# Kernel tuning notes

Hardware: AMD Instinct MI355X
Metric: run time of the kernel (lower is better)

The kernel has to match this reference:

```python
import jax, jax.numpy as jnp
import numpy as np

N_HEADS = 8
NEG_INF = -1e9


def setup_inputs() -> dict:
    key = jax.random.key(0)
    ks = jax.random.split(key, 9)
    B, S, D = 4, 2048, 512
    scale = 1.0 / np.sqrt(D)
    x = jax.random.normal(ks[0], (B, S, D), dtype=jnp.float32)
    mask = jnp.tril(jnp.ones((S, S), dtype=bool))[None, None, :, :]  # causal [1,1,S,S]
    W_Q_w = jax.random.normal(ks[1], (D, D), dtype=jnp.float32) * scale
    W_Q_b = jax.random.normal(ks[2], (D,), dtype=jnp.float32) * 0.02
    W_K_w = jax.random.normal(ks[3], (D, D), dtype=jnp.float32) * scale
    W_K_b = jax.random.normal(ks[4], (D,), dtype=jnp.float32) * 0.02
    W_V_w = jax.random.normal(ks[5], (D, D), dtype=jnp.float32) * scale
    W_V_b = jax.random.normal(ks[6], (D,), dtype=jnp.float32) * 0.02
    W_O_w = jax.random.normal(ks[7], (D, D), dtype=jnp.float32) * scale
    W_O_b = jax.random.normal(ks[8], (D,), dtype=jnp.float32) * 0.02
    return {"x": x, "mask": mask,
            "W_Q_w": W_Q_w, "W_Q_b": W_Q_b, "W_K_w": W_K_w, "W_K_b": W_K_b,
            "W_V_w": W_V_w, "W_V_b": W_V_b, "W_O_w": W_O_w, "W_O_b": W_O_b}


def reference(x, mask, W_Q_w, W_Q_b, W_K_w, W_K_b, W_V_w, W_V_b, W_O_w, W_O_b):
    B, S, D = x.shape
    H = N_HEADS
    Dh = D // H
    # projections (torch Linear: x @ W.T + b), split heads -> [B,H,S,Dh]
    def split_heads(t):
        return t.reshape(B, S, H, Dh).transpose(0, 2, 1, 3)
    Q = split_heads(x @ W_Q_w.T + W_Q_b)
    K = split_heads(x @ W_K_w.T + W_K_b)
    V = split_heads(x @ W_V_w.T + W_V_b)
    # scaled dot-product attention with explicit [B,H,S,S] scores
    scores = jnp.einsum("bhqd,bhkd->bhqk", Q, K) / jnp.sqrt(jnp.float32(Dh))
    scores = jnp.where(mask, scores, jnp.float32(NEG_INF))
    att = jax.nn.softmax(scores, axis=-1)
    out = jnp.einsum("bhqk,bhkd->bhqd", att, V)
    out = out.transpose(0, 2, 1, 3).reshape(B, S, D)
    return out @ W_O_w.T + W_O_b
```

## Files before the change

kernel.cpp:

```cpp
#include <hip/hip_runtime.h>
#include <hip/hip_bf16.h>

#define BATCH 4
#define SEQ   2048
#define DIM   512
#define NH    8
#define DH    64
#define NTOK  (BATCH*SEQ)

typedef __bf16 bf16x8 __attribute__((ext_vector_type(8)));
typedef float  f32x4  __attribute__((ext_vector_type(4)));

#define MFMA16(a,b,c) __builtin_amdgcn_mfma_f32_16x16x32_bf16((a),(b),(c),0,0,0)

#if __has_builtin(__builtin_amdgcn_exp2f)
#define EXP2F(x) __builtin_amdgcn_exp2f(x)
#else
#define EXP2F(x) exp2f(x)
#endif

#define QSCALE 0.18033688011112042f
#define SMAX 16.0f

typedef __attribute__((address_space(1))) void GAS;
typedef __attribute__((address_space(3))) void LAS;
__device__ __forceinline__ void gl_lds16(const void* g, void* l) {
  __builtin_amdgcn_global_load_lds((GAS*)g, (LAS*)l, 16, 0, 0);
}

__global__ __launch_bounds__(256) void cvt_f32_bf16(const float* __restrict__ src,
                                                    __bf16* __restrict__ dst, int n8) {
  int i = blockIdx.x * blockDim.x + threadIdx.x;
  if (i >= n8) return;
  const float4* s = (const float4*)src;
  float4 a = s[2*i], b = s[2*i+1];
  bf16x8 o;
  o[0] = (__bf16)a.x; o[1] = (__bf16)a.y; o[2] = (__bf16)a.z; o[3] = (__bf16)a.w;
  o[4] = (__bf16)b.x; o[5] = (__bf16)b.y; o[6] = (__bf16)b.z; o[7] = (__bf16)b.w;
  *(bf16x8*)&dst[8*i] = o;
}

__global__ __launch_bounds__(256) void cvt_weights(
    const float* __restrict__ s0, const float* __restrict__ s1,
    const float* __restrict__ s2, const float* __restrict__ s3,
    __bf16* __restrict__ o0, __bf16* __restrict__ o1,
    __bf16* __restrict__ o2, __bf16* __restrict__ o3) {
  int i = blockIdx.x * blockDim.x + threadIdx.x;
  const int which = i >> 15, off = i & 32767;
  const float* src = (which == 0) ? s0 : (which == 1) ? s1 : (which == 2) ? s2 : s3;
  __bf16* dst      = (which == 0) ? o0 : (which == 1) ? o1 : (which == 2) ? o2 : o3;
  const float4* s = (const float4*)src;
  float4 a = s[2*off], b = s[2*off+1];
  bf16x8 o;
  o[0] = (__bf16)a.x; o[1] = (__bf16)a.y; o[2] = (__bf16)a.z; o[3] = (__bf16)a.w;
  o[4] = (__bf16)b.x; o[5] = (__bf16)b.y; o[6] = (__bf16)b.z; o[7] = (__bf16)b.w;
  *(bf16x8*)&dst[8*off] = o;
}

__global__ __launch_bounds__(256) void gemm_qkv(
    const __bf16* __restrict__ xb,
    const __bf16* __restrict__ wq, const __bf16* __restrict__ wk,
    const __bf16* __restrict__ wv,
    const float* __restrict__ bq, const float* __restrict__ bk,
    const float* __restrict__ bv,
    __bf16* __restrict__ Qb, __bf16* __restrict__ Kb, __bf16* __restrict__ Vt)
{
  const int z = blockIdx.z;
  const __bf16* W    = (z == 0) ? wq : (z == 1) ? wk : wv;
  const float*  bias = (z == 0) ? bq : (z == 1) ? bk : bv;

  __shared__ __align__(16) __bf16 As[128*64];
  __shared__ __align__(16) __bf16 Bs[128*64];

  const int tid  = threadIdx.x;
  const int m0   = blockIdx.x * 128, n0 = blockIdx.y * 128;
  const int w    = tid >> 6, lane = tid & 63, quad = lane >> 4, l16 = lane & 15;
  const int wm   = (w >> 1) * 64, wn = (w & 1) * 64;
  const int srow = w*32 + (lane >> 3);
  const int scc  = (lane & 7) * 8;

  f32x4 acc[4][4] = {};

  for (int k0 = 0; k0 < DIM; k0 += 64) {
#pragma unroll
    for (int i = 0; i < 4; ++i) {
      const int row = srow + i*8;
      gl_lds16(&xb[(size_t)(m0+row)*DIM + k0 + scc], &As[(w*4+i)*512]);
      gl_lds16(&W [(size_t)(n0+row)*DIM + k0 + scc], &Bs[(w*4+i)*512]);
    }
    __syncthreads();
#pragma unroll
    for (int kk = 0; kk < 2; ++kk) {
      const int ko = kk*32 + quad*8;
      bf16x8 af[4], bfr[4];
#pragma unroll
      for (int f = 0; f < 4; ++f) {
        af[f]  = *(const bf16x8*)&As[(wm + f*16 + l16)*64 + ko];
        bfr[f] = *(const bf16x8*)&Bs[(wn + f*16 + l16)*64 + ko];
      }
#pragma unroll
      for (int fm = 0; fm < 4; ++fm)
#pragma unroll
        for (int fn = 0; fn < 4; ++fn)
          acc[fm][fn] = MFMA16(af[fm], bfr[fn], acc[fm][fn]);
    }
    __syncthreads();
  }

#pragma unroll
  for (int fm = 0; fm < 4; ++fm) {
#pragma unroll
    for (int fn = 0; fn < 4; ++fn) {
      const int col  = n0 + wn + fn*16 + l16;
      const float bc = bias[col];
      const int h = col >> 6, dh = col & 63;
#pragma unroll
      for (int r = 0; r < 4; ++r) {
        const int row = m0 + wm + fm*16 + quad*4 + r;
        const int b = row >> 11, s = row & 2047;
        const float v = acc[fm][fn][r] + bc;
        if (z == 2) {
          Vt[((size_t)(b*NH + h)*DH + dh)*SEQ + s] = (__bf16)v;
        } else if (z == 0) {
          Qb[((size_t)(b*NH + h)*SEQ + s)*DH + dh] = (__bf16)(v * QSCALE);
        } else {
          Kb[((size_t)(b*NH + h)*SEQ + s)*DH + dh] = (__bf16)v;
        }
      }
    }
  }
}

__global__ __launch_bounds__(256) void gemm_out(
    const __bf16* __restrict__ attnb, const __bf16* __restrict__ wo,
    const float* __restrict__ bo, float* __restrict__ out)
{
  __shared__ __align__(16) __bf16 As[128*64];
  __shared__ __align__(16) __bf16 Bs[128*64];

  const int tid = threadIdx.x;
  const int m0  = blockIdx.x * 128, n0 = blockIdx.y * 128;
  const int w   = tid >> 6, lane = tid & 63, quad = lane >> 4, l16 = lane & 15;
  const int wm  = (w >> 1) * 64, wn = (w & 1) * 64;
  const int srow = w*32 + (lane >> 3);
  const int scc  = (lane & 7) * 8;

  f32x4 acc[4][4] = {};

  for (int k0 = 0; k0 < DIM; k0 += 64) {
#pragma unroll
    for (int i = 0; i < 4; ++i) {
      const int row = srow + i*8;
      gl_lds16(&attnb[(size_t)(m0+row)*DIM + k0 + scc], &As[(w*4+i)*512]);
      gl_lds16(&wo   [(size_t)(n0+row)*DIM + k0 + scc], &Bs[(w*4+i)*512]);
    }
    __syncthreads();
#pragma unroll
    for (int kk = 0; kk < 2; ++kk) {
      const int ko = kk*32 + quad*8;
      bf16x8 af[4], bfr[4];
#pragma unroll
      for (int f = 0; f < 4; ++f) {
        af[f]  = *(const bf16x8*)&As[(wm + f*16 + l16)*64 + ko];
        bfr[f] = *(const bf16x8*)&Bs[(wn + f*16 + l16)*64 + ko];
      }
#pragma unroll
      for (int fm = 0; fm < 4; ++fm)
#pragma unroll
        for (int fn = 0; fn < 4; ++fn)
          acc[fm][fn] = MFMA16(af[fm], bfr[fn], acc[fm][fn]);
    }
    __syncthreads();
  }

#pragma unroll
  for (int fm = 0; fm < 4; ++fm) {
#pragma unroll
    for (int fn = 0; fn < 4; ++fn) {
      const int col  = n0 + wn + fn*16 + l16;
      const float bc = bo[col];
#pragma unroll
      for (int r = 0; r < 4; ++r) {
        const int row = m0 + wm + fm*16 + quad*4 + r;
        out[(size_t)row*DIM + col] = acc[fm][fn][r] + bc;
      }
    }
  }
}

__global__ __launch_bounds__(64) void flash_attn(
    const __bf16* __restrict__ Qb, const __bf16* __restrict__ Kb,
    const __bf16* __restrict__ Vt, __bf16* __restrict__ attnb)
{
  const int idx = blockIdx.x;
  const int bh  = idx & 31;
  const int t   = 63 - (idx >> 5);
  const int b   = bh >> 3, h = bh & 7;
  const int lane = threadIdx.x & 63, quad = lane >> 4, l16 = lane & 15;
  const int q0  = t * 32;

  const __bf16* Qp = Qb + (size_t)bh * SEQ * DH;
  const __bf16* Kp = Kb + (size_t)bh * SEQ * DH;
  const __bf16* Vp = Vt + (size_t)bh * DH * SEQ;

  __shared__ __align__(16) __bf16 Pw[32*88];

  bf16x8 qf[2][2];
#pragma unroll
  for (int mf = 0; mf < 2; ++mf)
#pragma unroll
    for (int kk = 0; kk < 2; ++kk)
      qf[mf][kk] = *(const bf16x8*)&Qp[(size_t)(q0 + mf*16 + l16)*DH + kk*32 + quad*8];

  f32x4 of[2][4] = {};
  float l_[2][4];
#pragma unroll
  for (int mf = 0; mf < 2; ++mf)
#pragma unroll
    for (int r = 0; r < 4; ++r) l_[mf][r] = 0.f;

  const int ktiles = (q0 >> 6) + 1;

  bf16x8 kfA[4][2], kfB[4][2];
#pragma unroll
  for (int fn = 0; fn < 4; ++fn)
#pragma unroll
    for (int kk = 0; kk < 2; ++kk)
      kfA[fn][kk] = *(const bf16x8*)&Kp[(size_t)(fn*16 + l16)*DH + kk*32 + quad*8];

#define TILE_STEP(KC, KN, KT)                                                  \
  {                                                                            \
    const int k0 = (KT) * 64;                                                  \
                   \
    bf16x8 vf[4][2];                                                           \
    _Pragma("unroll")                                                          \
    for (int nd = 0; nd < 4; ++nd)                                             \
      _Pragma("unroll")                                                        \
      for (int kq = 0; kq < 2; ++kq)                                           \
        vf[nd][kq] = *(const bf16x8*)&Vp[(size_t)(nd*16 + l16)*SEQ + k0 +      \
                                         kq*32 + quad*8];                      \
                               \
    {                                                                          \
      const int kn0 = ((KT) + 1 < ktiles) ? k0 + 64 : 0;                       \
      _Pragma("unroll")                                                        \
      for (int fn = 0; fn < 4; ++fn)                                           \
        _Pragma("unroll")                                                      \
        for (int kk = 0; kk < 2; ++kk)                                         \
          KN[fn][kk] = *(const bf16x8*)&Kp[(size_t)(kn0 + fn*16 + l16)*DH +    \
                                           kk*32 + quad*8];                    \
    }                                                                          \
                                   \
    f32x4 sf[2][4] = {};                                                       \
    __builtin_amdgcn_s_setprio(1);                                             \
    _Pragma("unroll")                                                          \
    for (int mf = 0; mf < 2; ++mf)                                             \
      _Pragma("unroll")                                                        \
      for (int fn = 0; fn < 4; ++fn) {                                         \
        sf[mf][fn] = MFMA16(qf[mf][0], KC[fn][0], sf[mf][fn]);                 \
        sf[mf][fn] = MFMA16(qf[mf][1], KC[fn][1], sf[mf][fn]);                 \
      }                                                                        \
    __builtin_amdgcn_s_setprio(0);                                             \
                               \
    if (k0 + 63 > q0) {                                                        \
      _Pragma("unroll")                                                        \
      for (int mf = 0; mf < 2; ++mf)                                           \
        _Pragma("unroll")                                                      \
        for (int fn = 0; fn < 4; ++fn) {                                       \
          const int col = k0 + fn*16 + l16;                                    \
          _Pragma("unroll")                                                    \
          for (int r = 0; r < 4; ++r) {                                        \
            const int row = q0 + mf*16 + quad*4 + r;                           \
            if (col > row) sf[mf][fn][r] = -1e30f;                             \
          }                                                                    \
        }                                                                      \
    }                                                                          \
                         \
    _Pragma("unroll")                                                          \
    for (int mf = 0; mf < 2; ++mf)                                             \
      _Pragma("unroll")                                                        \
      for (int fn = 0; fn < 4; ++fn)                                           \
        _Pragma("unroll")                                                      \
        for (int r = 0; r < 4; ++r)                                            \
          sf[mf][fn][r] = EXP2F(sf[mf][fn][r] - SMAX);                         \
    _Pragma("unroll")                                                          \
    for (int mf = 0; mf < 2; ++mf)                                             \
      _Pragma("unroll")                                                        \
      for (int r = 0; r < 4; ++r)                                              \
        l_[mf][r] += (sf[mf][0][r] + sf[mf][1][r]) +                           \
                     (sf[mf][2][r] + sf[mf][3][r]);                            \
                                           \
    _Pragma("unroll")                                                          \
    for (int mf = 0; mf < 2; ++mf)                                             \
      _Pragma("unroll")                                                        \
      for (int fn = 0; fn < 4; ++fn)                                           \
        _Pragma("unroll")                                                      \
        for (int r = 0; r < 4; ++r)                                            \
          Pw[(mf*16 + quad*4 + r)*88 + fn*16 + l16] = (__bf16)sf[mf][fn][r];   \
    bf16x8 pa[2][2];                                                           \
    _Pragma("unroll")                                                          \
    for (int mf = 0; mf < 2; ++mf)                                             \
      _Pragma("unroll")                                                        \
      for (int kq = 0; kq < 2; ++kq)                                           \
        pa[mf][kq] = *(const bf16x8*)&Pw[(mf*16 + l16)*88 + kq*32 + quad*8];   \
                                                      \
    __builtin_amdgcn_s_setprio(1);                                             \
    _Pragma("unroll")                                                          \
    for (int mf = 0; mf < 2; ++mf)                                             \
      _Pragma("unroll")                                                        \
      for (int nd = 0; nd < 4; ++nd) {                                         \
        of[mf][nd] = MFMA16(pa[mf][0], vf[nd][0], of[mf][nd]);                 \
        of[mf][nd] = MFMA16(pa[mf][1], vf[nd][1], of[mf][nd]);                 \
      }                                                                        \
    __builtin_amdgcn_s_setprio(0);                                             \
  }

  for (int kt = 0; kt < ktiles; kt += 2) {
    TILE_STEP(kfA, kfB, kt);
    if (kt + 1 < ktiles) TILE_STEP(kfB, kfA, kt + 1);
  }
#undef TILE_STEP

#pragma unroll
  for (int d = 1; d < 16; d <<= 1)
#pragma unroll
    for (int mf = 0; mf < 2; ++mf)
#pragma unroll
      for (int r = 0; r < 4; ++r)
        l_[mf][r] += __shfl_xor(l_[mf][r], d);
#pragma unroll
  for (int mf = 0; mf < 2; ++mf)
#pragma unroll
    for (int r = 0; r < 4; ++r)
      l_[mf][r] = 1.0f / l_[mf][r];
#pragma unroll
  for (int mf = 0; mf < 2; ++mf)
#pragma unroll
    for (int nd = 0; nd < 4; ++nd) {
      const int dh = nd*16 + l16;
#pragma unroll
      for (int r = 0; r < 4; ++r) {
        const int q = q0 + mf*16 + quad*4 + r;
        attnb[((size_t)b*SEQ + q)*DIM + h*DH + dh] = (__bf16)(of[mf][nd][r] * l_[mf][r]);
      }
    }
}

extern "C" void kernel_launch(void* const* d_in, const int* in_sizes, int n_in,
                              void* d_out, int out_size, void* d_ws, size_t ws_size,
                              hipStream_t stream) {
  const float* x  = (const float*)d_in[0];
  const float* Wq = (const float*)d_in[2];
  const float* bq = (const float*)d_in[3];
  const float* Wk = (const float*)d_in[4];
  const float* bk = (const float*)d_in[5];
  const float* Wv = (const float*)d_in[6];
  const float* bv = (const float*)d_in[7];
  const float* Wo = (const float*)d_in[8];
  const float* bo = (const float*)d_in[9];
  float* out = (float*)d_out;

  __bf16* xb    = (__bf16*)d_ws;
  __bf16* wq    = xb + (size_t)NTOK*DIM;
  __bf16* wk    = wq + DIM*DIM;
  __bf16* wv    = wk + DIM*DIM;
  __bf16* wo    = wv + DIM*DIM;
  __bf16* Qb    = wo + DIM*DIM;
  __bf16* Kb    = Qb + (size_t)NTOK*DIM;
  __bf16* Vt    = Kb + (size_t)NTOK*DIM;
  __bf16* attnb = Vt + (size_t)NTOK*DIM;

  cvt_f32_bf16<<<(NTOK*DIM/8)/256, 256, 0, stream>>>(x, xb, NTOK*DIM/8);
  cvt_weights<<<(4*DIM*DIM/8)/256, 256, 0, stream>>>(Wq, Wk, Wv, Wo, wq, wk, wv, wo);

  gemm_qkv<<<dim3(NTOK/128, DIM/128, 3), 256, 0, stream>>>(
      xb, wq, wk, wv, bq, bk, bv, Qb, Kb, Vt);

  flash_attn<<<2048, 64, 0, stream>>>(Qb, Kb, Vt, attnb);

  gemm_out<<<dim3(NTOK/128, DIM/128), 256, 0, stream>>>(attnb, wo, bo, out);
}
```

Measured before the change: 214.1 us.

## Split long causal query tiles across two KV-range blocks with atomic merge

```diff
diff --git a/kernel.cpp b/kernel.cpp
--- a/kernel.cpp
+++ b/kernel.cpp
@@ -9,6 +9,7 @@
 #define NTOK  (BATCH*SEQ)
 
 typedef __bf16 bf16x8 __attribute__((ext_vector_type(8)));
+typedef __bf16 bf16x4 __attribute__((ext_vector_type(4)));
 typedef float  f32x4  __attribute__((ext_vector_type(4)));
 
 #define MFMA16(a,b,c) __builtin_amdgcn_mfma_f32_16x16x32_bf16((a),(b),(c),0,0,0)
@@ -190,14 +191,32 @@
 
 __global__ __launch_bounds__(64) void flash_attn(
     const __bf16* __restrict__ Qb, const __bf16* __restrict__ Kb,
-    const __bf16* __restrict__ Vt, __bf16* __restrict__ attnb)
+    const __bf16* __restrict__ Vt, __bf16* __restrict__ attnb,
+    float* __restrict__ Of, float* __restrict__ Lb)
 {
   const int idx = blockIdx.x;
   const int bh  = idx & 31;
-  const int t   = 63 - (idx >> 5);
   const int b   = bh >> 3, h = bh & 7;
   const int lane = threadIdx.x & 63, quad = lane >> 4, l16 = lane & 15;
-  const int q0  = t * 32;
+
+  int t, c0tile, c1tile;
+  bool split;
+  if (idx < 2048) {
+    t = 63 - (idx >> 6);
+    const int ktiles = (t >> 1) + 1;
+    const int half   = ktiles >> 1;
+    const int c      = (idx >> 5) & 1;
+    c0tile = c ? half : 0;
+    c1tile = c ? ktiles : half;
+    split  = true;
+  } else {
+    const int li = idx - 2048;
+    t = 31 - (li >> 5);
+    c0tile = 0;
+    c1tile = (t >> 1) + 1;
+    split  = false;
+  }
+  const int q0 = t * 32;
 
   const __bf16* Qp = Qb + (size_t)bh * SEQ * DH;
   const __bf16* Kp = Kb + (size_t)bh * SEQ * DH;
@@ -219,14 +238,12 @@
 #pragma unroll
     for (int r = 0; r < 4; ++r) l_[mf][r] = 0.f;
 
-  const int ktiles = (q0 >> 6) + 1;
-
   bf16x8 kfA[4][2], kfB[4][2];
 #pragma unroll
   for (int fn = 0; fn < 4; ++fn)
 #pragma unroll
     for (int kk = 0; kk < 2; ++kk)
-      kfA[fn][kk] = *(const bf16x8*)&Kp[(size_t)(fn*16 + l16)*DH + kk*32 + quad*8];
+      kfA[fn][kk] = *(const bf16x8*)&Kp[(size_t)(c0tile*64 + fn*16 + l16)*DH + kk*32 + quad*8];
 
 #define TILE_STEP(KC, KN, KT)                                                  \
   {                                                                            \
@@ -241,7 +258,7 @@
                                          kq*32 + quad*8];                      \
                                \
     {                                                                          \
-      const int kn0 = ((KT) + 1 < ktiles) ? k0 + 64 : 0;                       \
+      const int kn0 = ((KT) + 1 < c1tile) ? k0 + 64 : 0;                       \
       _Pragma("unroll")                                                        \
       for (int fn = 0; fn < 4; ++fn)                                           \
         _Pragma("unroll")                                                      \
@@ -314,9 +331,9 @@
     __builtin_amdgcn_s_setprio(0);                                             \
   }
 
-  for (int kt = 0; kt < ktiles; kt += 2) {
+  for (int kt = c0tile; kt < c1tile; kt += 2) {
     TILE_STEP(kfA, kfB, kt);
-    if (kt + 1 < ktiles) TILE_STEP(kfB, kfA, kt + 1);
+    if (kt + 1 < c1tile) TILE_STEP(kfB, kfA, kt + 1);
   }
 #undef TILE_STEP
 
@@ -327,22 +344,62 @@
 #pragma unroll
       for (int r = 0; r < 4; ++r)
         l_[mf][r] += __shfl_xor(l_[mf][r], d);
-#pragma unroll
-  for (int mf = 0; mf < 2; ++mf)
-#pragma unroll
-    for (int r = 0; r < 4; ++r)
-      l_[mf][r] = 1.0f / l_[mf][r];
-#pragma unroll
-  for (int mf = 0; mf < 2; ++mf)
-#pragma unroll
-    for (int nd = 0; nd < 4; ++nd) {
-      const int dh = nd*16 + l16;
-#pragma unroll
-      for (int r = 0; r < 4; ++r) {
-        const int q = q0 + mf*16 + quad*4 + r;
-        attnb[((size_t)b*SEQ + q)*DIM + h*DH + dh] = (__bf16)(of[mf][nd][r] * l_[mf][r]);
-      }
-    }
+
+  if (!split) {
+#pragma unroll
+    for (int mf = 0; mf < 2; ++mf)
+#pragma unroll
+      for (int r = 0; r < 4; ++r)
+        l_[mf][r] = 1.0f / l_[mf][r];
+#pragma unroll
+    for (int mf = 0; mf < 2; ++mf)
+#pragma unroll
+      for (int nd = 0; nd < 4; ++nd) {
+        const int dh = nd*16 + l16;
+#pragma unroll
+        for (int r = 0; r < 4; ++r) {
+          const int q = q0 + mf*16 + quad*4 + r;
+          attnb[((size_t)b*SEQ + q)*DIM + h*DH + dh] = (__bf16)(of[mf][nd][r] * l_[mf][r]);
+        }
+      }
+  } else {
+    const int ro = (bh << 10) + (q0 - 1024);
+    if (l16 == 0) {
+#pragma unroll
+      for (int mf = 0; mf < 2; ++mf)
+#pragma unroll
+        for (int r = 0; r < 4; ++r)
+          atomicAdd(&Lb[ro + mf*16 + quad*4 + r], l_[mf][r]);
+    }
+#pragma unroll
+    for (int mf = 0; mf < 2; ++mf)
+#pragma unroll
+      for (int nd = 0; nd < 4; ++nd) {
+        const int dh = nd*16 + l16;
+#pragma unroll
+        for (int r = 0; r < 4; ++r)
+          atomicAdd(&Of[(size_t)(ro + mf*16 + quad*4 + r)*DH + dh], of[mf][nd][r]);
+      }
+  }
+}
+
+__global__ __launch_bounds__(256) void norm_split(
+    const float* __restrict__ Of, const float* __restrict__ Lb,
+    __bf16* __restrict__ attnb)
+{
+  const int i = blockIdx.x * 256 + threadIdx.x;
+  const int e = i * 4;
+  const int bh  = e >> 16;
+  const int rem = e & 65535;
+  const int row = rem >> 6;
+  const int dh  = rem & 63;
+  const f32x4 v = *(const f32x4*)&Of[e];
+  const float inv = 1.0f / Lb[(bh << 10) + row];
+  bf16x4 o;
+  o[0] = (__bf16)(v[0] * inv); o[1] = (__bf16)(v[1] * inv);
+  o[2] = (__bf16)(v[2] * inv); o[3] = (__bf16)(v[3] * inv);
+  const int b = bh >> 3, h = bh & 7, q = 1024 + row;
+  *(bf16x4*)&attnb[((size_t)b*SEQ + q)*DIM + h*DH + dh] = o;
 }
 
 extern "C" void kernel_launch(void* const* d_in, const int* in_sizes, int n_in,
@@ -369,13 +426,21 @@
   __bf16* Vt    = Kb + (size_t)NTOK*DIM;
   __bf16* attnb = Vt + (size_t)NTOK*DIM;
 
+  float* Of = (float*)xb;
+  float* Lb = (float*)wq;
+
   cvt_f32_bf16<<<(NTOK*DIM/8)/256, 256, 0, stream>>>(x, xb, NTOK*DIM/8);
   cvt_weights<<<(4*DIM*DIM/8)/256, 256, 0, stream>>>(Wq, Wk, Wv, Wo, wq, wk, wv, wo);
 
   gemm_qkv<<<dim3(NTOK/128, DIM/128, 3), 256, 0, stream>>>(
       xb, wq, wk, wv, bq, bk, bv, Qb, Kb, Vt);
 
-  flash_attn<<<2048, 64, 0, stream>>>(Qb, Kb, Vt, attnb);
+  hipMemsetAsync(Of, 0, (size_t)32*1024*64*sizeof(float), stream);
+  hipMemsetAsync(Lb, 0, (size_t)32*1024*sizeof(float), stream);
+
+  flash_attn<<<3072, 64, 0, stream>>>(Qb, Kb, Vt, attnb, Of, Lb);
+
+  norm_split<<<2048, 256, 0, stream>>>(Of, Lb, attnb);
 
   gemm_out<<<dim3(NTOK/128, DIM/128), 256, 0, stream>>>(attnb, wo, bo, out);
 }
```

Measured after the change: 240.4 us. 1.12x slower.

## Stage QKV epilogue through LDS for coalesced stores, merge converts, shrink out-GEMM tile

Applied to the files above, without the earlier changes.

```diff
diff --git a/kernel.cpp b/kernel.cpp
--- a/kernel.cpp
+++ b/kernel.cpp
@@ -28,27 +28,25 @@
   __builtin_amdgcn_global_load_lds((GAS*)g, (LAS*)l, 16, 0, 0);
 }
 
-__global__ __launch_bounds__(256) void cvt_f32_bf16(const float* __restrict__ src,
-                                                    __bf16* __restrict__ dst, int n8) {
-  int i = blockIdx.x * blockDim.x + threadIdx.x;
-  if (i >= n8) return;
-  const float4* s = (const float4*)src;
-  float4 a = s[2*i], b = s[2*i+1];
-  bf16x8 o;
-  o[0] = (__bf16)a.x; o[1] = (__bf16)a.y; o[2] = (__bf16)a.z; o[3] = (__bf16)a.w;
-  o[4] = (__bf16)b.x; o[5] = (__bf16)b.y; o[6] = (__bf16)b.z; o[7] = (__bf16)b.w;
-  *(bf16x8*)&dst[8*i] = o;
-}
-
-__global__ __launch_bounds__(256) void cvt_weights(
+__global__ __launch_bounds__(256) void cvt_all(
+    const float* __restrict__ x,
     const float* __restrict__ s0, const float* __restrict__ s1,
     const float* __restrict__ s2, const float* __restrict__ s3,
+    __bf16* __restrict__ xb,
     __bf16* __restrict__ o0, __bf16* __restrict__ o1,
     __bf16* __restrict__ o2, __bf16* __restrict__ o3) {
-  int i = blockIdx.x * blockDim.x + threadIdx.x;
-  const int which = i >> 15, off = i & 32767;
-  const float* src = (which == 0) ? s0 : (which == 1) ? s1 : (which == 2) ? s2 : s3;
-  __bf16* dst      = (which == 0) ? o0 : (which == 1) ? o1 : (which == 2) ? o2 : o3;
+  const int i = blockIdx.x * 256 + threadIdx.x;
+  const float* src;
+  __bf16* dst;
+  int off;
+  if (i < 524288) {
+    src = x; dst = xb; off = i;
+  } else {
+    const int j = i - 524288;
+    const int which = j >> 15; off = j & 32767;
+    src = (which == 0) ? s0 : (which == 1) ? s1 : (which == 2) ? s2 : s3;
+    dst = (which == 0) ? o0 : (which == 1) ? o1 : (which == 2) ? o2 : o3;
+  }
   const float4* s = (const float4*)src;
   float4 a = s[2*off], b = s[2*off+1];
   bf16x8 o;
@@ -69,8 +67,9 @@
   const __bf16* W    = (z == 0) ? wq : (z == 1) ? wk : wv;
   const float*  bias = (z == 0) ? bq : (z == 1) ? bk : bv;
 
-  __shared__ __align__(16) __bf16 As[128*64];
-  __shared__ __align__(16) __bf16 Bs[128*64];
+  __shared__ __align__(16) __bf16 smem[128*152];
+  __bf16* As = smem;
+  __bf16* Bs = smem + 128*64;
 
   const int tid  = threadIdx.x;
   const int m0   = blockIdx.x * 128, n0 = blockIdx.y * 128;
@@ -107,26 +106,46 @@
     __syncthreads();
   }
 
+  __bf16* Cs = smem;
 #pragma unroll
   for (int fm = 0; fm < 4; ++fm) {
 #pragma unroll
     for (int fn = 0; fn < 4; ++fn) {
-      const int col  = n0 + wn + fn*16 + l16;
-      const float bc = bias[col];
-      const int h = col >> 6, dh = col & 63;
+      const int cl  = wn + fn*16 + l16;
+      const float bc = bias[n0 + cl];
 #pragma unroll
       for (int r = 0; r < 4; ++r) {
-        const int row = m0 + wm + fm*16 + quad*4 + r;
-        const int b = row >> 11, s = row & 2047;
-        const float v = acc[fm][fn][r] + bc;
-        if (z == 2) {
-          Vt[((size_t)(b*NH + h)*DH + dh)*SEQ + s] = (__bf16)v;
-        } else if (z == 0) {
-          Qb[((size_t)(b*NH + h)*SEQ + s)*DH + dh] = (__bf16)(v * QSCALE);
-        } else {
-          Kb[((size_t)(b*NH + h)*SEQ + s)*DH + dh] = (__bf16)v;
-        }
+        const int rl = wm + fm*16 + quad*4 + r;
+        float v = acc[fm][fn][r] + bc;
+        if (z == 0) v *= QSCALE;
+        Cs[rl*152 + cl] = (__bf16)v;
       }
+    }
+  }
+  __syncthreads();
+
+  if (z < 2) {
+    const int r  = tid >> 1, hh = tid & 1;
+    const int grow = m0 + r, b = grow >> 11, s = grow & 2047;
+    const int h  = (n0 >> 6) + hh;
+    __bf16* O = (z == 0) ? Qb : Kb;
+    __bf16* dst = O + ((size_t)(b*NH + h)*SEQ + s)*DH;
+    const __bf16* srcr = &Cs[r*152 + hh*64];
+#pragma unroll
+    for (int j = 0; j < 8; ++j)
+      *(bf16x8*)&dst[j*8] = *(const bf16x8*)&srcr[j*8];
+  } else {
+    const int c  = tid >> 1, hh = tid & 1;
+    const int col = n0 + c, h = col >> 6, dh = col & 63;
+    const int b  = m0 >> 11, sbase = (m0 & 2047) + hh*64;
+    __bf16* dst = Vt + ((size_t)(b*NH + h)*DH + dh)*SEQ + sbase;
+#pragma unroll
+    for (int j8 = 0; j8 < 8; ++j8) {
+      bf16x8 o;
+#pragma unroll
+      for (int e = 0; e < 8; ++e)
+        o[e] = Cs[(hh*64 + j8*8 + e)*152 + c];
+      *(bf16x8*)&dst[j8*8] = o;
     }
   }
 }
@@ -135,37 +154,40 @@
     const __bf16* __restrict__ attnb, const __bf16* __restrict__ wo,
     const float* __restrict__ bo, float* __restrict__ out)
 {
-  __shared__ __align__(16) __bf16 As[128*64];
+  __shared__ __align__(16) __bf16 As[64*64];
   __shared__ __align__(16) __bf16 Bs[128*64];
 
   const int tid = threadIdx.x;
-  const int m0  = blockIdx.x * 128, n0 = blockIdx.y * 128;
+  const int m0  = blockIdx.x * 64, n0 = blockIdx.y * 128;
   const int w   = tid >> 6, lane = tid & 63, quad = lane >> 4, l16 = lane & 15;
-  const int wm  = (w >> 1) * 64, wn = (w & 1) * 64;
-  const int srow = w*32 + (lane >> 3);
+  const int wm  = (w >> 1) * 32, wn = (w & 1) * 64;
+  const int srow = w*8 + (lane >> 3);
   const int scc  = (lane & 7) * 8;
 
-  f32x4 acc[4][4] = {};
+  f32x4 acc[2][4] = {};
 
   for (int k0 = 0; k0 < DIM; k0 += 64) {
 #pragma unroll
-    for (int i = 0; i < 4; ++i) {
-      const int row = srow + i*8;
-      gl_lds16(&attnb[(size_t)(m0+row)*DIM + k0 + scc], &As[(w*4+i)*512]);
-      gl_lds16(&wo   [(size_t)(n0+row)*DIM + k0 + scc], &Bs[(w*4+i)*512]);
-    }
+    for (int i = 0; i < 2; ++i)
+      gl_lds16(&attnb[(size_t)(m0 + srow + i*32)*DIM + k0 + scc],
+               &As[(i*4 + w)*512]);
+#pragma unroll
+    for (int i = 0; i < 4; ++i)
+      gl_lds16(&wo[(size_t)(n0 + srow + i*32)*DIM + k0 + scc],
+               &Bs[(i*4 + w)*512]);
     __syncthreads();
 #pragma unroll
     for (int kk = 0; kk < 2; ++kk) {
       const int ko = kk*32 + quad*8;
-      bf16x8 af[4], bfr[4];
-#pragma unroll
-      for (int f = 0; f < 4; ++f) {
+      bf16x8 af[2], bfr[4];
+#pragma unroll
+      for (int f = 0; f < 2; ++f)
         af[f]  = *(const bf16x8*)&As[(wm + f*16 + l16)*64 + ko];
+#pragma unroll
+      for (int f = 0; f < 4; ++f)
         bfr[f] = *(const bf16x8*)&Bs[(wn + f*16 + l16)*64 + ko];
-      }
-#pragma unroll
-      for (int fm = 0; fm < 4; ++fm)
+#pragma unroll
+      for (int fm = 0; fm < 2; ++fm)
 #pragma unroll
         for (int fn = 0; fn < 4; ++fn)
           acc[fm][fn] = MFMA16(af[fm], bfr[fn], acc[fm][fn]);
@@ -174,7 +196,7 @@
   }
 
 #pragma unroll
-  for (int fm = 0; fm < 4; ++fm) {
+  for (int fm = 0; fm < 2; ++fm) {
 #pragma unroll
     for (int fn = 0; fn < 4; ++fn) {
       const int col  = n0 + wn + fn*16 + l16;
@@ -369,13 +391,12 @@
   __bf16* Vt    = Kb + (size_t)NTOK*DIM;
   __bf16* attnb = Vt + (size_t)NTOK*DIM;
 
-  cvt_f32_bf16<<<(NTOK*DIM/8)/256, 256, 0, stream>>>(x, xb, NTOK*DIM/8);
-  cvt_weights<<<(4*DIM*DIM/8)/256, 256, 0, stream>>>(Wq, Wk, Wv, Wo, wq, wk, wv, wo);
+  cvt_all<<<2560, 256, 0, stream>>>(x, Wq, Wk, Wv, Wo, xb, wq, wk, wv, wo);
 
   gemm_qkv<<<dim3(NTOK/128, DIM/128, 3), 256, 0, stream>>>(
       xb, wq, wk, wv, bq, bk, bv, Qb, Kb, Vt);
 
   flash_attn<<<2048, 64, 0, stream>>>(Qb, Kb, Vt, attnb);
 
-  gemm_out<<<dim3(NTOK/128, DIM/128), 256, 0, stream>>>(attnb, wo, bo, out);
-}
+  gemm_out<<<dim3(NTOK/64, DIM/128), 256, 0, stream>>>(attnb, wo, bo, out);
+}
```

After: 200.2 us. -6.5%, faster.
